# Optimization experiments

Measured on AMD Instinct MI355X. Metric: run time of the kernel, lower is better.

## Reference

```python
import jax, jax.numpy as jnp
import numpy as np
from jax import lax

N_QUBITS = 8
N_BLOCKS = 5

_H = jnp.array([[1.0, 1.0], [1.0, -1.0]], dtype=jnp.complex64) / np.sqrt(2.0).astype(np.float32)
# torchquantum PauliY.diagonalizing_gates = [Z, S, H] applied in order -> matrix H @ S @ Z = H @ diag(1, -1j)
_YROT = _H @ jnp.diag(jnp.array([1.0, -1j], dtype=jnp.complex64))


def apply_gate(st, U, wires):
    # st: [N, 2, 2, ..., 2] (n_qubits trailing axes); U: [2^k, 2^k]
    k = len(wires)
    axes = [w + 1 for w in wires]
    s = jnp.moveaxis(st, axes, list(range(1, k + 1)))
    shp = s.shape
    s = s.reshape(shp[0], 2 ** k, -1)
    s = jnp.einsum('ij,bjr->bir', U, s)
    return jnp.moveaxis(s.reshape(shp), list(range(1, k + 1)), axes)


def u3_mat(th, ph, lam):
    c = jnp.cos(0.5 * th).astype(jnp.complex64)
    s = jnp.sin(0.5 * th).astype(jnp.complex64)
    el = jnp.exp(1j * lam)
    ep = jnp.exp(1j * ph)
    return jnp.stack([jnp.stack([c, -el * s]), jnp.stack([ep * s, ep * el * c])])


def cu3_mat(th, ph, lam):
    M = jnp.eye(4, dtype=jnp.complex64)
    return M.at[2:, 2:].set(u3_mat(th, ph, lam))


def z_expvals(st):
    # <Z_w> for every wire from marginal probabilities
    n = st.ndim - 1
    mag = st.real ** 2 + st.imag ** 2
    outs = []
    for w in range(n):
        axes = tuple(a for a in range(1, n + 1) if a != w + 1)
        p = mag.sum(axes)  # [N, 2]
        outs.append(p[:, 0] - p[:, 1])
    return jnp.stack(outs, axis=1)


def quantum_conv(x, conv_w, conv_b, u3_params, cu3_params, fc_w, fc_b):
    n = N_QUBITS
    B, C, H, W = x.shape
    y = lax.conv_general_dilated(x, conv_w, (1, 1), 'SAME',
                                 dimension_numbers=('NCHW', 'OIHW', 'NCHW'))
    y = y + conv_b[None, :, None, None]
    ang = y.transpose(0, 2, 3, 1).reshape(-1, n)  # [B*H*W, n_qubits]
    Npx = ang.shape[0]
    # RY(theta)|0> encoding: product state of [cos(t/2), sin(t/2)] per wire
    c = jnp.cos(0.5 * ang)
    s = jnp.sin(0.5 * ang)
    st = jnp.stack([c[:, 0], s[:, 0]], axis=1).astype(jnp.complex64)
    for w in range(1, n):
        q = jnp.stack([c[:, w], s[:, w]], axis=1).astype(jnp.complex64)
        st = (st[:, :, None] * q[:, None, :]).reshape(Npx, -1)
    st = st.reshape((Npx,) + (2,) * n)
    # U3CU3Layer0: per block, U3 on each wire then circular CU3 ring
    for b in range(N_BLOCKS):
        for w in range(n):
            st = apply_gate(st, u3_mat(u3_params[b, w, 0], u3_params[b, w, 1], u3_params[b, w, 2]), [w])
        for w in range(n):
            st = apply_gate(st, cu3_mat(cu3_params[b, w, 0], cu3_params[b, w, 1], cu3_params[b, w, 2]), [w, (w + 1) % n])
    # MeasureAll(Z), then MeasureAll(X) and MeasureAll(Y) which MUTATE the device
    # state with their diagonalizing gates (torchquantum semantics)
    mz = z_expvals(st)
    for w in range(n):
        st = apply_gate(st, _H, [w])
    mx = z_expvals(st)
    for w in range(n):
        st = apply_gate(st, _YROT, [w])
    my = z_expvals(st)
    meas = jnp.concatenate([mz, mx, my], axis=1)  # [B*H*W, 3*n]
    out = meas @ fc_w.T + fc_b
    return out.reshape(B, H, W, -1).transpose(0, 3, 1, 2)


def setup_inputs() -> dict:
    key = jax.random.key(0)
    ks = jax.random.split(key, 7)
    n, cin, cout = N_QUBITS, 16, 32
    x = jax.random.normal(ks[0], (4, cin, 64, 64), dtype=jnp.float32)
    conv_w = jax.random.normal(ks[1], (n, cin, 3, 3), dtype=jnp.float32) / np.sqrt(cin * 9)
    conv_b = jax.random.normal(ks[2], (n,), dtype=jnp.float32) * 0.01
    u3_params = jax.random.uniform(ks[3], (N_BLOCKS, n, 3), dtype=jnp.float32, minval=-np.pi, maxval=np.pi)
    cu3_params = jax.random.uniform(ks[4], (N_BLOCKS, n, 3), dtype=jnp.float32, minval=-np.pi, maxval=np.pi)
    fc_w = jax.random.normal(ks[5], (cout, 3 * n), dtype=jnp.float32) / np.sqrt(3 * n)
    fc_b = jax.random.normal(ks[6], (cout,), dtype=jnp.float32) * 0.01
    return {'x': x, 'conv_w': conv_w, 'conv_b': conv_b, 'u3_params': u3_params,
            'cu3_params': cu3_params, 'fc_w': fc_w, 'fc_b': fc_b}


def reference(x, conv_w, conv_b, u3_params, cu3_params, fc_w, fc_b):
    return quantum_conv(x, conv_w, conv_b, u3_params, cu3_params, fc_w, fc_b)
```

## Files before the change

### kernel.cpp

```cpp
#include <hip/hip_runtime.h>

typedef float v2f __attribute__((ext_vector_type(2)));

template<int C>
__device__ __forceinline__ float dppmov(float x) {
  return __int_as_float(__builtin_amdgcn_update_dpp(0, __float_as_int(x), C, 0xF, 0xF, true));
}
template<int IMM>
__device__ __forceinline__ float dswz(float x) {
  return __int_as_float(__builtin_amdgcn_ds_swizzle(__float_as_int(x), IMM));
}
__device__ __forceinline__ float bperm(float x, int a) {
  return __int_as_float(__builtin_amdgcn_ds_bpermute(a, __float_as_int(x)));
}
template<int M>
__device__ __forceinline__ float bfly(float x) {
  if constexpr (M == 1)      return dppmov<0xB1>(x);
  else if constexpr (M == 2) return dppmov<0x4E>(x);
  else if constexpr (M == 8) return dppmov<0x128>(x);
  else                       return dswz<0x101F>(x);
}
template<int M>
__device__ __forceinline__ v2f bfly2(v2f v) {
  v2f o; o.x = bfly<M>(v.x); o.y = bfly<M>(v.y); return o;
}
__device__ __forceinline__ v2f sp(float s) { v2f v; v.x = s; v.y = s; return v; }
__device__ __forceinline__ v2f vfma(v2f a, v2f b, v2f c) {
  return __builtin_elementwise_fma(a, b, c);
}

template<int M, int CM>
__device__ __forceinline__ void crossG(v2f Sr[16], v2f Si[16],
    const float* __restrict__ g, int lane) {
  const bool hi = (lane & M) != 0;
  float fr, fi, gr, gi;
  if constexpr (CM == 0) {
    fr = hi ? g[6] : g[0]; fi = hi ? g[7] : g[1];
    gr = hi ? g[4] : g[2]; gi = hi ? g[5] : g[3];
  } else {
    const bool ct = (lane & CM) != 0;
    float f0r = hi ? g[6]  : g[0],  f0i = hi ? g[7]  : g[1];
    float g0r = hi ? g[4]  : g[2],  g0i = hi ? g[5]  : g[3];
    float f1r = hi ? g[14] : g[8],  f1i = hi ? g[15] : g[9];
    float g1r = hi ? g[12] : g[10], g1i = hi ? g[13] : g[11];
    fr = ct ? f1r : f0r; fi = ct ? f1i : f0i;
    gr = ct ? g1r : g0r; gi = ct ? g1i : g0i;
  }
  v2f vfr = sp(fr), vfi = sp(fi), vgr = sp(gr), vgi = sp(gi);
  v2f vfiN = sp(-fi), vgiN = sp(-gi);
#pragma unroll
  for (int r = 0; r < 16; ++r) {
    v2f pR = bfly2<M>(Sr[r]);
    v2f pI = bfly2<M>(Si[r]);
    v2f nR = vfma(vgiN, pI, vfma(vgr, pR, vfma(vfiN, Si[r], vfr * Sr[r])));
    v2f nI = vfma(vgi,  pR, vfma(vgr, pI, vfma(vfi,  Sr[r], vfr * Si[r])));
    Sr[r] = nR; Si[r] = nI;
  }
}

__device__ __forceinline__ void mixP(v2f& x0r, v2f& x0i, v2f& x1r, v2f& x1i,
    float m0r, float m0i, float m1r, float m1i,
    float m2r, float m2i, float m3r, float m3i) {
  v2f n0r = vfma(sp(-m1i), x1i, vfma(sp(m1r), x1r, vfma(sp(-m0i), x0i, sp(m0r) * x0r)));
  v2f n0i = vfma(sp( m1i), x1r, vfma(sp(m1r), x1i, vfma(sp( m0i), x0r, sp(m0r) * x0i)));
  v2f n1r = vfma(sp(-m3i), x1i, vfma(sp(m3r), x1r, vfma(sp(-m2i), x0i, sp(m2r) * x0r)));
  v2f n1i = vfma(sp( m3i), x1r, vfma(sp(m3r), x1i, vfma(sp( m2i), x0r, sp(m2r) * x0i)));
  x0r = n0r; x0i = n0i; x1r = n1r; x1i = n1i;
}

__device__ __forceinline__ void f4N(v2f Sr[16], v2f Si[16],
    const float* __restrict__ g, int lane) {
  const bool ct = (lane & 1) != 0;
  float m[8];
#pragma unroll
  for (int jj = 0; jj < 8; ++jj) m[jj] = ct ? g[8 + jj] : g[jj];
#pragma unroll
  for (int r = 0; r < 8; ++r)
    mixP(Sr[r], Si[r], Sr[r + 8], Si[r + 8],
         m[0], m[1], m[2], m[3], m[4], m[5], m[6], m[7]);
}
__device__ __forceinline__ void f5N(v2f Sr[16], v2f Si[16],
    const float* __restrict__ g) {
#pragma unroll
  for (int r = 0; r < 4; ++r)
    mixP(Sr[r], Si[r], Sr[r + 4], Si[r + 4],
         g[0], g[1], g[2], g[3], g[4], g[5], g[6], g[7]);
#pragma unroll
  for (int r = 8; r < 12; ++r)
    mixP(Sr[r], Si[r], Sr[r + 4], Si[r + 4],
         g[8], g[9], g[10], g[11], g[12], g[13], g[14], g[15]);
}
__device__ __forceinline__ void f6N(v2f Sr[16], v2f Si[16],
    const float* __restrict__ g) {
#pragma unroll
  for (int t = 0; t < 4; ++t) {
    const int r0 = (t >> 1) * 8 + (t & 1);
    mixP(Sr[r0], Si[r0], Sr[r0 + 2], Si[r0 + 2],
         g[0], g[1], g[2], g[3], g[4], g[5], g[6], g[7]);
    const int r1 = r0 + 4;
    mixP(Sr[r1], Si[r1], Sr[r1 + 2], Si[r1 + 2],
         g[8], g[9], g[10], g[11], g[12], g[13], g[14], g[15]);
  }
}
__device__ __forceinline__ void f7N(v2f Sr[16], v2f Si[16],
    const float* __restrict__ g) {
#pragma unroll
  for (int t = 0; t < 4; ++t) {
    const int r0 = t * 4;
    mixP(Sr[r0], Si[r0], Sr[r0 + 1], Si[r0 + 1],
         g[0], g[1], g[2], g[3], g[4], g[5], g[6], g[7]);
    const int r1 = r0 + 2;
    mixP(Sr[r1], Si[r1], Sr[r1 + 1], Si[r1 + 1],
         g[8], g[9], g[10], g[11], g[12], g[13], g[14], g[15]);
  }
}
__device__ __forceinline__ void f8pN(v2f Sr[16], v2f Si[16],
    const float* __restrict__ g, int lane) {
  const bool hi = (lane & 8) != 0;
  float fr[2], fi[2], gr[2], gi[2];
  fr[0] = hi ? g[6]  : g[0];  fi[0] = hi ? g[7]  : g[1];
  gr[0] = hi ? g[4]  : g[2];  gi[0] = hi ? g[5]  : g[3];
  fr[1] = hi ? g[14] : g[8];  fi[1] = hi ? g[15] : g[9];
  gr[1] = hi ? g[12] : g[10]; gi[1] = hi ? g[13] : g[11];
#pragma unroll
  for (int r = 0; r < 16; ++r) {
    const int m = r & 1;
    v2f pR = bfly2<8>(Sr[r]);
    v2f pI = bfly2<8>(Si[r]);
    v2f nR = vfma(sp(-gi[m]), pI, vfma(sp(gr[m]), pR, vfma(sp(-fi[m]), Si[r], sp(fr[m]) * Sr[r])));
    v2f nI = vfma(sp( gi[m]), pR, vfma(sp(gr[m]), pI, vfma(sp( fi[m]), Sr[r], sp(fr[m]) * Si[r])));
    Sr[r] = nR; Si[r] = nI;
  }
}
__device__ __forceinline__ void f8N(v2f Sr[16], v2f Si[16],
    const float* __restrict__ g, int lane) {
  const bool hi = (lane & 8) != 0;
  const float fr = hi ? g[6] : g[0], fi = hi ? g[7] : g[1];
  const float gr = hi ? g[4] : g[2], gi = hi ? g[5] : g[3];
#pragma unroll
  for (int r = 1; r < 16; r += 2) {
    v2f pR = bfly2<8>(Sr[r]);
    v2f pI = bfly2<8>(Si[r]);
    v2f nR = vfma(sp(-gi), pI, vfma(sp(gr), pR, vfma(sp(-fi), Si[r], sp(fr) * Sr[r])));
    v2f nI = vfma(sp( gi), pR, vfma(sp(gr), pI, vfma(sp( fi), Sr[r], sp(fr) * Si[r])));
    Sr[r] = nR; Si[r] = nI;
  }
}

template<int M>
__device__ __forceinline__ void crossO(const v2f Sr[16], const v2f Si[16],
                                       v2f& re, v2f& im) {
  v2f r = sp(0.0f), i = sp(0.0f);
#pragma unroll
  for (int k = 0; k < 16; ++k) {
    v2f pr = bfly2<M>(Sr[k]);
    v2f pi = bfly2<M>(Si[k]);
    r = vfma(Sr[k], pr, r);
    r = vfma(Si[k], pi, r);
    i = vfma(Si[k], pr, i);
    i = vfma(-Sr[k], pi, i);
  }
  re = r; im = i;
}

__device__ __forceinline__ void mm2(const float* A, const float* B, float* D) {
  D[0] = A[0]*B[0] - A[1]*B[1] + A[2]*B[4] - A[3]*B[5];
  D[1] = A[0]*B[1] + A[1]*B[0] + A[2]*B[5] + A[3]*B[4];
  D[2] = A[0]*B[2] - A[1]*B[3] + A[2]*B[6] - A[3]*B[7];
  D[3] = A[0]*B[3] + A[1]*B[2] + A[2]*B[7] + A[3]*B[6];
  D[4] = A[4]*B[0] - A[5]*B[1] + A[6]*B[4] - A[7]*B[5];
  D[5] = A[4]*B[1] + A[5]*B[0] + A[6]*B[5] + A[7]*B[4];
  D[6] = A[4]*B[2] - A[5]*B[3] + A[6]*B[6] - A[7]*B[7];
  D[7] = A[4]*B[3] + A[5]*B[2] + A[6]*B[7] + A[7]*B[6];
}
__device__ __forceinline__ void u3fill(const float* src, float* o) {
  float th = src[0], ph = src[1], lam = src[2];
  float c = cosf(0.5f * th), s = sinf(0.5f * th);
  float cl = cosf(lam), sl = sinf(lam);
  float cp = cosf(ph), spv = sinf(ph);
  float cpl = cosf(ph + lam), spl = sinf(ph + lam);
  o[0] = c;        o[1] = 0.0f;
  o[2] = -cl * s;  o[3] = -sl * s;
  o[4] = cp * s;   o[5] = spv * s;
  o[6] = cpl * c;  o[7] = spl * c;
}

__global__ __launch_bounds__(128) void prep_kernel(
    const float* __restrict__ u3p, const float* __restrict__ cu3p,
    const float* __restrict__ fcw, float* __restrict__ G,
    float* __restrict__ FCW3) {
  __shared__ float Us[40][8];
  __shared__ float Cs[40][8];
  int t = threadIdx.x;
  if (t < 40) u3fill(u3p + t * 3, Us[t]);
  if (t >= 64 && t < 104) u3fill(cu3p + (t - 64) * 3, Cs[t - 64]);
  __syncthreads();
  if (t == 0) {
#pragma unroll
    for (int j = 0; j < 8; ++j) G[j] = Us[0][j];
  } else if (t < 36) {
    int j = t - 1, b = j / 7, k = j % 7;
    float* dst = G + 8 + b * 112 + k * 16;
    const float* U = Us[b * 8 + k + 1];
    const float* C = Cs[b * 8 + k];
#pragma unroll
    for (int q = 0; q < 8; ++q) dst[q] = U[q];
    mm2(C, U, dst + 8);
  } else if (t < 40) {
    int b = t - 36;
    float* dst = G + 568 + b * 16;
    const float* U = Us[(b + 1) * 8];
    const float* C = Cs[b * 8 + 7];
#pragma unroll
    for (int q = 0; q < 8; ++q) dst[q] = U[q];
    mm2(U, C, dst + 8);
  } else if (t == 40) {
#pragma unroll
    for (int j = 0; j < 8; ++j) G[632 + j] = Cs[39][j];
  }
  for (int i = t; i < 768; i += 128) {
    int tt = i % 24;
    int stage = tt >> 3, w = tt & 7;
    float sc = (stage >= 1 && w >= 4) ? 2.0f : 1.0f;
    FCW3[i] = fcw[i] * sc;
  }
}

__global__ __launch_bounds__(256) void qconv_kernel(
    const float* __restrict__ x, const float* __restrict__ cw,
    const float* __restrict__ cb, const float* __restrict__ G,
    const float* __restrict__ FCW3, const float* __restrict__ fcb,
    float* __restrict__ out) {
  const int lane = threadIdx.x & 63;
  const int wid = __builtin_amdgcn_readfirstlane(
      (int)((blockIdx.x * blockDim.x + threadIdx.x) >> 6));
  const int p0 = wid * 8;
  const int q = lane & 15;

  float ang;
  {
    const int px = lane >> 3;
    const int oc = lane & 7;
    const int p  = p0 + px;
    const int b  = p >> 12;
    const int hh = (p >> 6) & 63;
    const int wim = p & 63;
    float acc = cb[oc];
#pragma unroll 4
    for (int ic = 0; ic < 16; ++ic) {
      const float* wp = cw + (oc * 16 + ic) * 9;
      const float* xp = x + (b * 16 + ic) * 4096;
#pragma unroll
      for (int kh = 0; kh < 3; ++kh) {
        int ih = hh + kh - 1;
        bool rok = (unsigned)ih < 64u;
        int ihc = rok ? ih : 0;
#pragma unroll
        for (int kw = 0; kw < 3; ++kw) {
          int iw = wim + kw - 1;
          bool ok = rok && ((unsigned)iw < 64u);
          int iwc = ((unsigned)iw < 64u) ? iw : 0;
          float xv = xp[ihc * 64 + iwc];
          acc = fmaf(ok ? xv : 0.0f, wp[kh * 3 + kw], acc);
        }
      }
    }
    ang = acc;
  }

  v2f Sr[16], Si[16];
  {
    const int gb = (lane & 48) << 2;
    float aA[8], aB[8];
#pragma unroll
    for (int w = 0; w < 8; ++w) {
      aA[w] = bperm(ang, gb + (w << 2));
      aB[w] = bperm(ang, gb + ((8 + w) << 2));
    }
    float cA[8], sA[8], cB[8], sB[8];
#pragma unroll
    for (int w = 0; w < 8; ++w) {
      __sincosf(0.5f * aA[w], &sA[w], &cA[w]);
      __sincosf(0.5f * aB[w], &sB[w], &cB[w]);
    }
    v2f c0; c0.x = cA[0]; c0.y = cB[0];
    v2f s0; s0.x = sA[0]; s0.y = sB[0];
    v2f c0r = vfma(sp(G[2]), s0, sp(G[0]) * c0);
    v2f c0i = vfma(sp(G[3]), s0, sp(G[1]) * c0);
    v2f s0r = vfma(sp(G[6]), s0, sp(G[4]) * c0);
    v2f s0i = vfma(sp(G[7]), s0, sp(G[5]) * c0);
    const bool w0 = (q & 8) != 0;
    v2f selR = w0 ? s0r : c0r;
    v2f selI = w0 ? s0i : c0i;
    float fA = ((q & 4) ? sA[1] : cA[1]) * ((q & 2) ? sA[2] : cA[2])
             * ((q & 1) ? sA[3] : cA[3]);
    float fB = ((q & 4) ? sB[1] : cB[1]) * ((q & 2) ? sB[2] : cB[2])
             * ((q & 1) ? sB[3] : cB[3]);
    v2f uu[4], vv[4];
    uu[0].x = cA[6]*cA[7]; uu[1].x = cA[6]*sA[7];
    uu[2].x = sA[6]*cA[7]; uu[3].x = sA[6]*sA[7];
    uu[0].y = cB[6]*cB[7]; uu[1].y = cB[6]*sB[7];
    uu[2].y = sB[6]*cB[7]; uu[3].y = sB[6]*sB[7];
    float vA0 = fA * cA[4], vA1 = fA * sA[4];
    float vB0 = fB * cB[4], vB1 = fB * sB[4];
    vv[0].x = vA0*cA[5]; vv[1].x = vA0*sA[5];
    vv[2].x = vA1*cA[5]; vv[3].x = vA1*sA[5];
    vv[0].y = vB0*cB[5]; vv[1].y = vB0*sB[5];
    vv[2].y = vB1*cB[5]; vv[3].y = vB1*sB[5];
#pragma unroll
    for (int r = 0; r < 16; ++r) {
      v2f base = vv[r >> 2] * uu[r & 3];
      Sr[r] = selR * base;
      Si[r] = selI * base;
    }
  }

  for (int b = 0; b < 5; ++b) {
    const float* base = G + 8 + b * 112;
    crossG<4, 8>(Sr, Si, base +  0, lane);
    crossG<2, 4>(Sr, Si, base + 16, lane);
    crossG<1, 2>(Sr, Si, base + 32, lane);
    f4N(Sr, Si, base + 48, lane);
    f5N(Sr, Si, base + 64);
    f6N(Sr, Si, base + 80);
    f7N(Sr, Si, base + 96);
    if (b < 4) f8pN(Sr, Si, G + 568 + b * 16, lane);
  }
  f8N(Sr, Si, G + 632, lane);

  float sg[4];
  sg[0] = (q & 8) ? -1.0f : 1.0f;
  sg[1] = (q & 4) ? -1.0f : 1.0f;
  sg[2] = (q & 2) ? -1.0f : 1.0f;
  sg[3] = (q & 1) ? -1.0f : 1.0f;

  v2f PT[24];
  {
    v2f re0, im0, re1, im1, re2, im2, re3, im3;
    crossO<8>(Sr, Si, re0, im0);
    crossO<4>(Sr, Si, re1, im1);
    crossO<2>(Sr, Si, re2, im2);
    crossO<1>(Sr, Si, re3, im3);
    PT[8]  = re0; PT[9]  = re1; PT[10] = re2; PT[11] = re3;
    PT[16] = sp(sg[0]) * im0; PT[17] = sp(sg[1]) * im1;
    PT[18] = sp(sg[2]) * im2; PT[19] = sp(sg[3]) * im3;

    v2f P[16];
#pragma unroll
    for (int r = 0; r < 16; ++r) P[r] = vfma(Si[r], Si[r], Sr[r] * Sr[r]);
    v2f t01[8];
#pragma unroll
    for (int k = 0; k < 8; ++k) t01[k] = P[2*k] + P[2*k+1];
    v2f q0 = t01[0] + t01[1], q1 = t01[2] + t01[3];
    v2f q2 = t01[4] + t01[5], q3 = t01[6] + t01[7];
    v2f h0 = q0 + q1, h1 = q2 + q3;
    v2f p  = h0 + h1;
    PT[4] = h0 - h1;
    PT[5] = (q0 - q1) + (q2 - q3);
    PT[6] = (t01[0]-t01[1]) + (t01[2]-t01[3])
          + (t01[4]-t01[5]) + (t01[6]-t01[7]);
    PT[7] = (P[0]-P[1]) + (P[2]-P[3]) + (P[4]-P[5]) + (P[6]-P[7])
          + (P[8]-P[9]) + (P[10]-P[11]) + (P[12]-P[13]) + (P[14]-P[15]);
    PT[0] = sp(sg[0]) * p; PT[1] = sp(sg[1]) * p;
    PT[2] = sp(sg[2]) * p; PT[3] = sp(sg[3]) * p;

    v2f re, im;
    re = sp(0.0f); im = sp(0.0f);
#pragma unroll
    for (int r = 0; r < 8; ++r) {
      re = vfma(Sr[r], Sr[r+8], re); re = vfma(Si[r], Si[r+8], re);
      im = vfma(Si[r], Sr[r+8], im); im = vfma(-Sr[r], Si[r+8], im);
    }
    PT[12] = re; PT[20] = im;
    re = sp(0.0f); im = sp(0.0f);
#pragma unroll
    for (int t = 0; t < 8; ++t) {
      const int lo = (t & 3) + (t >> 2) * 8;
      re = vfma(Sr[lo], Sr[lo+4], re); re = vfma(Si[lo], Si[lo+4], re);
      im = vfma(Si[lo], Sr[lo+4], im); im = vfma(-Sr[lo], Si[lo+4], im);
    }
    PT[13] = re; PT[21] = im;
    re = sp(0.0f); im = sp(0.0f);
#pragma unroll
    for (int t = 0; t < 8; ++t) {
      const int lo = (t & 1) + (t >> 1) * 4;
      re = vfma(Sr[lo], Sr[lo+2], re); re = vfma(Si[lo], Si[lo+2], re);
      im = vfma(Si[lo], Sr[lo+2], im); im = vfma(-Sr[lo], Si[lo+2], im);
    }
    PT[14] = re; PT[22] = im;
    re = sp(0.0f); im = sp(0.0f);
#pragma unroll
    for (int t = 0; t < 8; ++t) {
      const int lo = 2 * t;
      re = vfma(Sr[lo], Sr[lo+1], re); re = vfma(Si[lo], Si[lo+1], re);
      im = vfma(Si[lo], Sr[lo+1], im); im = vfma(-Sr[lo], Si[lo+1], im);
    }
    PT[15] = re; PT[23] = im;
  }

  const int j = q & 7;
  const bool isB = (q & 8) != 0;
  float mm[24];
#pragma unroll
  for (int t = 0; t < 24; ++t) {
    v2f v = PT[t] + bfly2<8>(PT[t]);
    float s = isB ? v.y : v.x;
    s += bfly<1>(s);
    s += bfly<2>(s);
    s += bfly<4>(s);
    mm[t] = s;
  }

  const int g = lane >> 4;
  const int p = p0 + 2 * g + (isB ? 1 : 0);
  const int ob = (p >> 12) * 131072 + (p & 4095);
#pragma unroll
  for (int k = 0; k < 4; ++k) {
    const int ch = 4 * j + k;
    const float4* w4 = reinterpret_cast<const float4*>(FCW3 + ch * 24);
    float acc = fcb[ch];
#pragma unroll
    for (int u = 0; u < 6; ++u) {
      float4 tv = w4[u];
      acc = fmaf(mm[u*4+0], tv.x, acc);
      acc = fmaf(mm[u*4+1], tv.y, acc);
      acc = fmaf(mm[u*4+2], tv.z, acc);
      acc = fmaf(mm[u*4+3], tv.w, acc);
    }
    out[ob + ch * 4096] = acc;
  }
}

extern "C" void kernel_launch(void* const* d_in, const int* in_sizes, int n_in,
                              void* d_out, int out_size, void* d_ws, size_t ws_size,
                              hipStream_t stream) {
  const float* x      = (const float*)d_in[0];
  const float* conv_w = (const float*)d_in[1];
  const float* conv_b = (const float*)d_in[2];
  const float* u3p    = (const float*)d_in[3];
  const float* cu3p   = (const float*)d_in[4];
  const float* fcw    = (const float*)d_in[5];
  const float* fcb    = (const float*)d_in[6];
  float* out = (float*)d_out;

  float* ws   = (float*)d_ws;
  float* G    = ws;
  float* FCW3 = ws + 640;

  prep_kernel<<<1, 128, 0, stream>>>(u3p, cu3p, fcw, G, FCW3);
  qconv_kernel<<<512, 256, 0, stream>>>(x, conv_w, conv_b, G, FCW3, fcb, out);
}
```

Baseline: 114.5 us.

## Fuse gate-matrix prep kernel into main kernel and stage coefficients in LDS

Drops the separate single-block prep kernel. Each block of the main kernel now computes the fused U3/CU3 gate coefficients and the scaled FC weights into shared memory, and the gate and FC reads come from LDS instead of global memory. This removes one kernel launch and the serialization between the two kernels. In exchange every block repeats the trig prep work, adds two barriers, and loses the scalar/constant-cache loads of uniform coefficients (LDS reads replace SMEM loads, and __restrict__ is dropped).

Measured after the change: 107.0 us. 1.07x faster.

```diff
diff --git a/kernel.cpp b/kernel.cpp
--- a/kernel.cpp
+++ b/kernel.cpp
@@ -31,7 +31,7 @@
 
 template<int M, int CM>
 __device__ __forceinline__ void crossG(v2f Sr[16], v2f Si[16],
-    const float* __restrict__ g, int lane) {
+    const float* g, int lane) {
   const bool hi = (lane & M) != 0;
   float fr, fi, gr, gi;
   if constexpr (CM == 0) {
@@ -69,7 +69,7 @@
 }
 
 __device__ __forceinline__ void f4N(v2f Sr[16], v2f Si[16],
-    const float* __restrict__ g, int lane) {
+    const float* g, int lane) {
   const bool ct = (lane & 1) != 0;
   float m[8];
 #pragma unroll
@@ -79,8 +79,7 @@
     mixP(Sr[r], Si[r], Sr[r + 8], Si[r + 8],
          m[0], m[1], m[2], m[3], m[4], m[5], m[6], m[7]);
 }
-__device__ __forceinline__ void f5N(v2f Sr[16], v2f Si[16],
-    const float* __restrict__ g) {
+__device__ __forceinline__ void f5N(v2f Sr[16], v2f Si[16], const float* g) {
 #pragma unroll
   for (int r = 0; r < 4; ++r)
     mixP(Sr[r], Si[r], Sr[r + 4], Si[r + 4],
@@ -90,8 +89,7 @@
     mixP(Sr[r], Si[r], Sr[r + 4], Si[r + 4],
          g[8], g[9], g[10], g[11], g[12], g[13], g[14], g[15]);
 }
-__device__ __forceinline__ void f6N(v2f Sr[16], v2f Si[16],
-    const float* __restrict__ g) {
+__device__ __forceinline__ void f6N(v2f Sr[16], v2f Si[16], const float* g) {
 #pragma unroll
   for (int t = 0; t < 4; ++t) {
     const int r0 = (t >> 1) * 8 + (t & 1);
@@ -102,8 +100,7 @@
          g[8], g[9], g[10], g[11], g[12], g[13], g[14], g[15]);
   }
 }
-__device__ __forceinline__ void f7N(v2f Sr[16], v2f Si[16],
-    const float* __restrict__ g) {
+__device__ __forceinline__ void f7N(v2f Sr[16], v2f Si[16], const float* g) {
 #pragma unroll
   for (int t = 0; t < 4; ++t) {
     const int r0 = t * 4;
@@ -115,7 +112,7 @@
   }
 }
 __device__ __forceinline__ void f8pN(v2f Sr[16], v2f Si[16],
-    const float* __restrict__ g, int lane) {
+    const float* g, int lane) {
   const bool hi = (lane & 8) != 0;
   float fr[2], fi[2], gr[2], gi[2];
   fr[0] = hi ? g[6]  : g[0];  fi[0] = hi ? g[7]  : g[1];
@@ -133,7 +130,7 @@
   }
 }
 __device__ __forceinline__ void f8N(v2f Sr[16], v2f Si[16],
-    const float* __restrict__ g, int lane) {
+    const float* g, int lane) {
   const bool hi = (lane & 8) != 0;
   const float fr = hi ? g[6] : g[0], fi = hi ? g[7] : g[1];
   const float gr = hi ? g[4] : g[2], gi = hi ? g[5] : g[3];
@@ -185,52 +182,53 @@
   o[6] = cpl * c;  o[7] = spl * c;
 }
 
-__global__ __launch_bounds__(128) void prep_kernel(
-    const float* __restrict__ u3p, const float* __restrict__ cu3p,
-    const float* __restrict__ fcw, float* __restrict__ G,
-    float* __restrict__ FCW3) {
+__global__ __launch_bounds__(256) void qconv_kernel(
+    const float* __restrict__ x, const float* __restrict__ cw,
+    const float* __restrict__ cb, const float* __restrict__ u3p,
+    const float* __restrict__ cu3p, const float* __restrict__ fcw,
+    const float* __restrict__ fcb, float* __restrict__ out) {
   __shared__ float Us[40][8];
   __shared__ float Cs[40][8];
-  int t = threadIdx.x;
-  if (t < 40) u3fill(u3p + t * 3, Us[t]);
-  if (t >= 64 && t < 104) u3fill(cu3p + (t - 64) * 3, Cs[t - 64]);
-  __syncthreads();
-  if (t == 0) {
-#pragma unroll
-    for (int j = 0; j < 8; ++j) G[j] = Us[0][j];
-  } else if (t < 36) {
-    int j = t - 1, b = j / 7, k = j % 7;
-    float* dst = G + 8 + b * 112 + k * 16;
-    const float* U = Us[b * 8 + k + 1];
-    const float* C = Cs[b * 8 + k];
-#pragma unroll
-    for (int q = 0; q < 8; ++q) dst[q] = U[q];
-    mm2(C, U, dst + 8);
-  } else if (t < 40) {
-    int b = t - 36;
-    float* dst = G + 568 + b * 16;
-    const float* U = Us[(b + 1) * 8];
-    const float* C = Cs[b * 8 + 7];
-#pragma unroll
-    for (int q = 0; q < 8; ++q) dst[q] = U[q];
-    mm2(U, C, dst + 8);
-  } else if (t == 40) {
-#pragma unroll
-    for (int j = 0; j < 8; ++j) G[632 + j] = Cs[39][j];
-  }
-  for (int i = t; i < 768; i += 128) {
-    int tt = i % 24;
-    int stage = tt >> 3, w = tt & 7;
-    float sc = (stage >= 1 && w >= 4) ? 2.0f : 1.0f;
-    FCW3[i] = fcw[i] * sc;
-  }
-}
-
-__global__ __launch_bounds__(256) void qconv_kernel(
-    const float* __restrict__ x, const float* __restrict__ cw,
-    const float* __restrict__ cb, const float* __restrict__ G,
-    const float* __restrict__ FCW3, const float* __restrict__ fcb,
-    float* __restrict__ out) {
+  __shared__ float Gs[640];
+  __shared__ float FCWs[768];
+
+  {
+    const int t = threadIdx.x;
+    if (t < 40) u3fill(u3p + t * 3, Us[t]);
+    if (t >= 64 && t < 104) u3fill(cu3p + (t - 64) * 3, Cs[t - 64]);
+    __syncthreads();
+    if (t == 0) {
+#pragma unroll
+      for (int j = 0; j < 8; ++j) Gs[j] = Us[0][j];
+    } else if (t < 36) {
+      int j = t - 1, b = j / 7, k = j % 7;
+      float* dst = Gs + 8 + b * 112 + k * 16;
+      const float* U = Us[b * 8 + k + 1];
+      const float* C = Cs[b * 8 + k];
+#pragma unroll
+      for (int u = 0; u < 8; ++u) dst[u] = U[u];
+      mm2(C, U, dst + 8);
+    } else if (t < 40) {
+      int b = t - 36;
+      float* dst = Gs + 568 + b * 16;
+      const float* U = Us[(b + 1) * 8];
+      const float* C = Cs[b * 8 + 7];
+#pragma unroll
+      for (int u = 0; u < 8; ++u) dst[u] = U[u];
+      mm2(U, C, dst + 8);
+    } else if (t == 40) {
+#pragma unroll
+      for (int j = 0; j < 8; ++j) Gs[632 + j] = Cs[39][j];
+    }
+    for (int i = t; i < 768; i += 256) {
+      int tt = i % 24;
+      int stage = tt >> 3, w = tt & 7;
+      float sc = (stage >= 1 && w >= 4) ? 2.0f : 1.0f;
+      FCWs[i] = fcw[i] * sc;
+    }
+    __syncthreads();
+  }
+
   const int lane = threadIdx.x & 63;
   const int wid = __builtin_amdgcn_readfirstlane(
       (int)((blockIdx.x * blockDim.x + threadIdx.x) >> 6));
@@ -285,10 +283,10 @@
     }
     v2f c0; c0.x = cA[0]; c0.y = cB[0];
     v2f s0; s0.x = sA[0]; s0.y = sB[0];
-    v2f c0r = vfma(sp(G[2]), s0, sp(G[0]) * c0);
-    v2f c0i = vfma(sp(G[3]), s0, sp(G[1]) * c0);
-    v2f s0r = vfma(sp(G[6]), s0, sp(G[4]) * c0);
-    v2f s0i = vfma(sp(G[7]), s0, sp(G[5]) * c0);
+    v2f c0r = vfma(sp(Gs[2]), s0, sp(Gs[0]) * c0);
+    v2f c0i = vfma(sp(Gs[3]), s0, sp(Gs[1]) * c0);
+    v2f s0r = vfma(sp(Gs[6]), s0, sp(Gs[4]) * c0);
+    v2f s0i = vfma(sp(Gs[7]), s0, sp(Gs[5]) * c0);
     const bool w0 = (q & 8) != 0;
     v2f selR = w0 ? s0r : c0r;
     v2f selI = w0 ? s0i : c0i;
@@ -316,7 +314,7 @@
   }
 
   for (int b = 0; b < 5; ++b) {
-    const float* base = G + 8 + b * 112;
+    const float* base = Gs + 8 + b * 112;
     crossG<4, 8>(Sr, Si, base +  0, lane);
     crossG<2, 4>(Sr, Si, base + 16, lane);
     crossG<1, 2>(Sr, Si, base + 32, lane);
@@ -324,9 +322,9 @@
     f5N(Sr, Si, base + 64);
     f6N(Sr, Si, base + 80);
     f7N(Sr, Si, base + 96);
-    if (b < 4) f8pN(Sr, Si, G + 568 + b * 16, lane);
-  }
-  f8N(Sr, Si, G + 632, lane);
+    if (b < 4) f8pN(Sr, Si, Gs + 568 + b * 16, lane);
+  }
+  f8N(Sr, Si, Gs + 632, lane);
 
   float sg[4];
   sg[0] = (q & 8) ? -1.0f : 1.0f;
@@ -417,16 +415,10 @@
 #pragma unroll
   for (int k = 0; k < 4; ++k) {
     const int ch = 4 * j + k;
-    const float4* w4 = reinterpret_cast<const float4*>(FCW3 + ch * 24);
+    const float* wr = FCWs + ch * 24;
     float acc = fcb[ch];
 #pragma unroll
-    for (int u = 0; u < 6; ++u) {
-      float4 tv = w4[u];
-      acc = fmaf(mm[u*4+0], tv.x, acc);
-      acc = fmaf(mm[u*4+1], tv.y, acc);
-      acc = fmaf(mm[u*4+2], tv.z, acc);
-      acc = fmaf(mm[u*4+3], tv.w, acc);
-    }
+    for (int u = 0; u < 24; ++u) acc = fmaf(mm[u], wr[u], acc);
     out[ob + ch * 4096] = acc;
   }
 }
@@ -443,10 +435,6 @@
   const float* fcb    = (const float*)d_in[6];
   float* out = (float*)d_out;
 
-  float* ws   = (float*)d_ws;
-  float* G    = ws;
-  float* FCW3 = ws + 640;
-
-  prep_kernel<<<1, 128, 0, stream>>>(u3p, cu3p, fcw, G, FCW3);
-  qconv_kernel<<<512, 256, 0, stream>>>(x, conv_w, conv_b, G, FCW3, fcb, out);
-}
+  qconv_kernel<<<512, 256, 0, stream>>>(x, conv_w, conv_b, u3p, cu3p,
+                                        fcw, fcb, out);
+}
```
